# Performance work log

Measured on AMD Instinct MI355X. Metric: run time of the kernel, lower is better.

The kernel has to match this reference:

```python
import jax, jax.numpy as jnp
import numpy as np

B, J, C = 256, 21, 256   # batch, joints, in_dim
H, D = 8, 256            # heads, out_dim (=hidden)
L, K = 2, 8              # layers, knn_k


def _knn_idx(coords, k):
    # coords: (B,J,3). Squared distances give same ordering as cdist p=2.
    d2 = jnp.sum((coords[:, :, None, :] - coords[:, None, :, :]) ** 2, axis=-1)  # (B,J,J)
    order = jnp.argsort(d2, axis=-1)
    return order[..., 1:k + 1]  # drop self -> (B,J,K)


def _mhgat(x, nbr_idx, wq, wk, wv, wp):
    b, j, _ = x.shape
    q = (x @ wq).reshape(b, j, H, D)
    k = (x @ wk).reshape(b, j, H, D)
    v = (x @ wv).reshape(b, j, H, D)
    bi = jnp.arange(b)[:, None, None]
    k_nbr = k[bi, nbr_idx]  # (B,J,K,H,D) gather of neighbor keys
    v_nbr = v[bi, nbr_idx]  # (B,J,K,H,D)
    attn = jnp.einsum('bjhd,bjkhd->bjkh', q, k_nbr) / np.float32(np.sqrt(D))
    attn = jax.nn.leaky_relu(attn, negative_slope=0.2)
    attn = jax.nn.softmax(attn, axis=2)  # over K neighbors
    out = jnp.einsum('bjkh,bjkhd->bjhd', attn, v_nbr).reshape(b, j, H * D)
    return out @ wp  # (B,J,hidden)


def setup_inputs() -> dict:
    key = jax.random.key(0)
    ks = jax.random.split(key, 9)
    s_in = 1.0 / np.sqrt(C)
    s_hd = 1.0 / np.sqrt(H * D)
    s_h = 1.0 / np.sqrt(D)
    joint_feats = jax.random.normal(ks[0], (B, J, C), jnp.float32)
    # layer-stacked weights (in_dim == hidden == 256 so both layers stack)
    wq = jax.random.normal(ks[1], (L, C, H * D), jnp.float32) * s_in
    wk = jax.random.normal(ks[2], (L, C, H * D), jnp.float32) * s_in
    wv = jax.random.normal(ks[3], (L, C, H * D), jnp.float32) * s_in
    wp = jax.random.normal(ks[4], (L, H * D, D), jnp.float32) * s_hd
    ws = jax.random.normal(ks[5], (L, C, D), jnp.float32) * s_in
    wskip0 = jax.random.normal(ks[6], (C, D), jnp.float32) * s_in
    fc_w = jax.random.normal(ks[7], (D, 3), jnp.float32) * s_h
    fc_b = jax.random.normal(ks[8], (3,), jnp.float32) * s_h
    return {"joint_feats": joint_feats, "wq": wq, "wk": wk, "wv": wv,
            "wp": wp, "ws": ws, "wskip0": wskip0, "fc_w": fc_w, "fc_b": fc_b}


def reference(joint_feats, wq, wk, wv, wp, ws, wskip0, fc_w, fc_b):
    h0 = joint_feats
    h = h0
    stats = []
    for l in range(L):
        nbr_idx = _knn_idx(jax.lax.stop_gradient(h[..., :3]), K)  # dynamic kNN graph
        out = _mhgat(h, nbr_idx, wq[l], wk[l], wv[l], wp[l])
        h = jax.nn.relu(out + h @ ws[l] + h0 @ wskip0)
        stats.append(jnp.abs(h).mean())
    coords = h @ fc_w + fc_b
    alphas = jnp.mean(jnp.stack(stats))
    return coords, alphas
```

## Files before the change

### kernel.cpp

```cpp
#include <hip/hip_runtime.h>
#include <hip/hip_bf16.h>
#include <math.h>
#include <type_traits>

namespace {
constexpr int Bb = 256, Jj = 21, Cc = 256, Hh = 8, Dd = 256;
constexpr int Mrows = Bb * Jj;
constexpr int HD    = Hh * Dd;
constexpr int QKVN  = 3 * HD;
constexpr int KNN   = 8;
constexpr int KFUSE = HD + Cc + Cc;

constexpr size_t OFF_QKV   = 0;
constexpr size_t OFF_T     = OFF_QKV   + (size_t)Mrows*QKVN*2;
constexpr size_t OFF_ATT   = OFF_T;
constexpr size_t OFF_GT    = OFF_T     + (size_t)Mrows*HD*4;
constexpr size_t OFF_JFB   = OFF_GT    + (size_t)HD*768*2;
constexpr size_t OFF_JFH   = OFF_JFB   + (size_t)Mrows*Cc*2;
constexpr size_t OFF_JFL   = OFF_JFH   + (size_t)Mrows*Cc*2;
constexpr size_t OFF_JFD   = OFF_JFL   + (size_t)Mrows*Cc*2;
constexpr size_t OFF_H1B   = OFF_JFD   + (size_t)Mrows*Cc*2;
constexpr size_t OFF_H2F   = OFF_H1B   + (size_t)Mrows*Cc*2;
constexpr size_t OFF_WQKVT = OFF_H2F   + (size_t)Mrows*Cc*4;
constexpr size_t OFF_FBT   = OFF_WQKVT + (size_t)2*QKVN*Cc*2;
constexpr size_t OFF_WVP   = OFF_FBT   + (size_t)2*Cc*KFUSE*2;
constexpr size_t OFF_VPROJ = OFF_WVP   + (size_t)Cc*24*4;
constexpr size_t OFF_WSUM  = OFF_VPROJ + (size_t)Mrows*24*4;
constexpr size_t OFF_CRD   = OFF_WSUM  + (size_t)Cc*4*4;
constexpr size_t OFF_NBR0  = OFF_CRD   + (size_t)Mrows*4*4;
constexpr size_t OFF_NBR1  = OFF_NBR0  + (size_t)Mrows*KNN*4;
constexpr size_t OFF_STAT  = OFF_NBR1  + (size_t)Mrows*KNN*4;
}

typedef short short8 __attribute__((ext_vector_type(8)));
typedef _Float16 half8 __attribute__((ext_vector_type(8)));
typedef _Float16 half4v __attribute__((ext_vector_type(4)));
typedef unsigned short u16x8 __attribute__((ext_vector_type(8)));
typedef float f32x4 __attribute__((ext_vector_type(4)));

__device__ __forceinline__ unsigned short f2bf(float x) {
    unsigned int u = __float_as_uint(x);
    u = u + 0x7fffu + ((u >> 16) & 1u);
    return (unsigned short)(u >> 16);
}
__device__ __forceinline__ float bf2f(unsigned short b) {
    return __uint_as_float(((unsigned int)b) << 16);
}

__device__ __forceinline__ void knn_body(int b, const float* __restrict__ src,
                                         int ld, int* __restrict__ nbr,
                                         float (*cs)[3]) {
    int t = threadIdx.x;
    if (t < Jj) {
        const float* p = src + (size_t)(b * Jj + t) * ld;
        cs[t][0] = p[0]; cs[t][1] = p[1]; cs[t][2] = p[2];
    }
    __syncthreads();
    if (t < Jj) {
        float x = cs[t][0], y = cs[t][1], z = cs[t][2];
        float d2[Jj];
        #pragma unroll
        for (int jj = 0; jj < Jj; ++jj) {
            float dx = x - cs[jj][0], dy = y - cs[jj][1], dz = z - cs[jj][2];
            d2[jj] = dx*dx + dy*dy + dz*dz;
        }
        unsigned int used = 0u;
        int out_base = (b * Jj + t) * KNN;
        #pragma unroll
        for (int r = 0; r <= KNN; ++r) {
            int best = -1; float bd = INFINITY;
            #pragma unroll
            for (int jj = 0; jj < Jj; ++jj)
                if (!((used >> jj) & 1u) && d2[jj] < bd) { bd = d2[jj]; best = jj; }
            used |= (1u << best);
            if (r > 0) nbr[out_base + r - 1] = best;
        }
    }
}

__global__ __launch_bounds__(256)
void mega_prep_kernel(const float* __restrict__ jf,
                      const float* __restrict__ wq, const float* __restrict__ wk,
                      const float* __restrict__ wv, const float* __restrict__ wp,
                      const float* __restrict__ wsw, const float* __restrict__ wsk,
                      unsigned short* __restrict__ wqkvT,
                      unsigned short* __restrict__ fbt, float* __restrict__ stats,
                      float* __restrict__ wsum,
                      unsigned short* __restrict__ jfb, _Float16* __restrict__ jfh,
                      _Float16* __restrict__ jfl, _Float16* __restrict__ jfd,
                      _Float16* __restrict__ GT, float* __restrict__ Wvp2,
                      int* __restrict__ nbr0) {
    __shared__ __align__(16) char sm[17408];
    int bid = blockIdx.x;
    int tidx = threadIdx.x;

    if (bid < 4352) {
        const float* src; unsigned short* dst;
        int ldin, ldout, tilesX, tile;
        constexpr size_t CH = (size_t)Cc * HD;
        if (bid < 3072) {
            int op = bid >> 9; tile = bid & 511; tilesX = 64;
            ldin = HD; ldout = Cc;
            const float* s3[3] = {wq, wk, wv};
            src = s3[op % 3] + (size_t)(op / 3) * CH;
            dst = wqkvT + (size_t)(op % 3) * HD * Cc + (size_t)(op / 3) * QKVN * Cc;
        } else if (bid < 4096) {
            int op = (bid - 3072) >> 9; tile = (bid - 3072) & 511; tilesX = 8;
            ldin = Cc; ldout = KFUSE;
            src = wp + (size_t)op * HD * Cc;
            dst = fbt + (size_t)op * Cc * KFUSE;
        } else {
            int q = bid - 4096; int op = q >> 6; tile = q & 63; tilesX = 8;
            ldin = Cc; ldout = KFUSE;
            const float* s4[4] = {wsw, wsw + (size_t)Cc * Cc, wsk, wsk};
            src = s4[op];
            dst = fbt + (size_t)(op & 1) * Cc * KFUSE + HD + (size_t)(op >> 1) * Cc;
        }
        int bx = tile % tilesX, by = tile / tilesX;
        int n0 = bx * 32, k0 = by * 32;
        float (*t)[33] = (float(*)[33])sm;
        int r = tidx >> 3, c4 = (tidx & 7) * 4;
        float4 v = *(const float4*)&src[(size_t)(k0 + r) * ldin + n0 + c4];
        t[r][c4+0] = v.x; t[r][c4+1] = v.y; t[r][c4+2] = v.z; t[r][c4+3] = v.w;
        __syncthreads();
        ushort4 o;
        o.x = f2bf(t[c4+0][r]); o.y = f2bf(t[c4+1][r]);
        o.z = f2bf(t[c4+2][r]); o.w = f2bf(t[c4+3][r]);
        *(ushort4*)&dst[(size_t)(n0 + r) * ldout + k0 + c4] = o;
    } else if (bid == 4352) {
        int e = tidx;
        float4 o;
        o.x = wsw[(size_t)e*Dd + 0] + wsk[(size_t)e*Dd + 0];
        o.y = wsw[(size_t)e*Dd + 1] + wsk[(size_t)e*Dd + 1];
        o.z = wsw[(size_t)e*Dd + 2] + wsk[(size_t)e*Dd + 2];
        o.w = 0.0f;
        *(float4*)&wsum[e*4] = o;
        if (e < 2) stats[e] = 0.0f;
    } else if (bid < 5697) {
        int i = (bid - 4353) * 256 + tidx;
        float4 v = ((const float4*)jf)[i];
        float x[4] = {v.x, v.y, v.z, v.w};
        ushort4 ob; half4v oh, ol, od;
        #pragma unroll
        for (int u = 0; u < 4; ++u) {
            ((unsigned short*)&ob)[u] = f2bf(x[u]);
            _Float16 h = (_Float16)x[u];
            oh[u] = h;
            ol[u] = (_Float16)((x[u] - (float)h) * 16.0f);
            od[u] = (_Float16)(x[u] * 0.0078125f);
        }
        ((ushort4*)jfb)[i] = ob;
        ((half4v*)jfh)[i] = oh;
        ((half4v*)jfl)[i] = ol;
        ((half4v*)jfd)[i] = od;
    } else if (bid < 5825) {
        int q = bid - 5697;
        int h = q >> 4, rem = q & 15;
        int m0 = (rem >> 2) * 64, n0 = (rem & 3) * 64;
        float (*As)[68] = (float(*)[68])sm;
        float (*Ws)[68] = (float(*)[68])(sm + 8704);
        int ty = tidx >> 4, tx = tidx & 15;
        float acc[4][4] = {};
        for (int kb = 0; kb < 256; kb += 32) {
            #pragma unroll
            for (int it = 0; it < 2; ++it) {
                int c = tidx + it * 256;
                int row = c >> 3, col = (c & 7) * 4;
                float4 v = *(const float4*)&wq[(size_t)(m0 + row)*HD + h*256 + kb + col];
                float4 u = *(const float4*)&wk[(size_t)(n0 + row)*HD + h*256 + kb + col];
                As[col+0][row] = v.x; As[col+1][row] = v.y;
                As[col+2][row] = v.z; As[col+3][row] = v.w;
                Ws[col+0][row] = u.x; Ws[col+1][row] = u.y;
                Ws[col+2][row] = u.z; Ws[col+3][row] = u.w;
            }
            __syncthreads();
            #pragma unroll
            for (int kk = 0; kk < 32; ++kk) {
                float4 a = *(const float4*)&As[kk][ty*4];
                float4 b = *(const float4*)&Ws[kk][tx*4];
                float av[4] = {a.x, a.y, a.z, a.w};
                float bv[4] = {b.x, b.y, b.z, b.w};
                #pragma unroll
                for (int i = 0; i < 4; ++i)
                    #pragma unroll
                    for (int j = 0; j < 4; ++j)
                        acc[i][j] += av[i] * bv[j];
            }
            __syncthreads();
        }
        #pragma unroll
        for (int j = 0; j < 4; ++j) {
            int n = h*256 + n0 + tx*4 + j;
            half4v hi, hs, lo;
            #pragma unroll
            for (int i = 0; i < 4; ++i) {
                float g = acc[i][j];
                _Float16 gh = (_Float16)g;
                hi[i] = gh;
                hs[i] = (_Float16)(g * 0.0625f);
                lo[i] = (_Float16)((g - (float)gh) * 128.0f);
            }
            _Float16* base = &GT[(size_t)n*768 + m0 + ty*4];
            *(half4v*)(base)       = hi;
            *(half4v*)(base + 256) = hs;
            *(half4v*)(base + 512) = lo;
        }
    } else if (bid < 5833) {
        int h = bid - 5825;
        float (*wpc)[3] = (float(*)[3])sm;
        int t = tidx;
        const float* p = &wp[(size_t)(h*256 + t) * Cc];
        wpc[t][0] = p[0]; wpc[t][1] = p[1]; wpc[t][2] = p[2];
        __syncthreads();
        const float* vr = &wv[(size_t)t*HD + h*256];
        float a0=0, a1=0, a2=0;
        for (int d = 0; d < 256; ++d) {
            float v = vr[d];
            a0 += v*wpc[d][0]; a1 += v*wpc[d][1]; a2 += v*wpc[d][2];
        }
        float* o = &Wvp2[(size_t)t*24 + h*3];
        o[0]=a0; o[1]=a1; o[2]=a2;
    } else {
        knn_body(bid - 5833, jf, Cc, nbr0, (float(*)[3])sm);
    }
}

template<int BM, int BN, int BK, int NSEG, bool RELU_STATS, bool OUT_BF16, bool F16>
__device__ __forceinline__
void gemm_core(unsigned short* As, unsigned short* Bs, float* red,
               int bm, int bn,
               const unsigned short* __restrict__ A0, int lda0, int klen0,
               const unsigned short* __restrict__ A1, int lda1, int klen1,
               const unsigned short* __restrict__ A2, int lda2, int klen2,
               const unsigned short* __restrict__ Bt, int ldb,
               void* __restrict__ Cv, int ldc, float* __restrict__ stat) {
    constexpr int WM = BM/2, WN = BN/2;
    constexpr int MW = WM/16, NW = WN/16, KW = BK/32;
    constexpr int CHUNKA = BM*BK/8;
    constexpr int CHUNKB = BN*BK/8;
    constexpr int KB8 = BK/8;
    constexpr int SWZ = KB8 - 1;
    using frag = std::conditional_t<F16, half8, short8>;

    int tid = threadIdx.x;
    int wid = tid >> 6, lane = tid & 63;
    int wr = wid >> 1, wc = wid & 1;

    f32x4 acc[MW][NW];
    #pragma unroll
    for (int m = 0; m < MW; ++m)
        #pragma unroll
        for (int n = 0; n < NW; ++n)
            acc[m][n] = (f32x4){0.f, 0.f, 0.f, 0.f};

    const unsigned short* Aseg[3] = {A0, A1, A2};
    const int ldas[3] = {lda0, lda1, lda2};
    const int klens[3] = {klen0, klen1, klen2};

    int kglob = 0;
    for (int seg = 0; seg < NSEG; ++seg) {
        const unsigned short* A = Aseg[seg];
        const int lda = ldas[seg];
        const int klen = klens[seg];
        for (int k0 = 0; k0 < klen; k0 += BK) {
            #pragma unroll
            for (int it = 0; it < CHUNKA/256; ++it) {
                int c = tid + it*256;
                int row = c / KB8;
                int kp = (c % KB8) ^ (row & SWZ);
                __builtin_amdgcn_global_load_lds(
                    (const __attribute__((address_space(1))) unsigned int*)
                        (A + (size_t)(bm + row)*lda + k0 + kp*8),
                    (__attribute__((address_space(3))) unsigned int*)(As + c*8),
                    16, 0, 0);
            }
            #pragma unroll
            for (int it = 0; it < CHUNKB/256; ++it) {
                int c = tid + it*256;
                int row = c / KB8;
                int kp = (c % KB8) ^ (row & SWZ);
                __builtin_amdgcn_global_load_lds(
                    (const __attribute__((address_space(1))) unsigned int*)
                        (Bt + (size_t)(bn + row)*ldb + kglob + k0 + kp*8),
                    (__attribute__((address_space(3))) unsigned int*)(Bs + c*8),
                    16, 0, 0);
            }
            __syncthreads();
            #pragma unroll
            for (int kp = 0; kp < KW; ++kp) {
                frag af[MW], bf[NW];
                int cbase = kp*4 + (lane >> 4);
                #pragma unroll
                for (int m = 0; m < MW; ++m) {
                    int r = wr*WM + m*16 + (lane & 15);
                    af[m] = *(const frag*)&As[r*BK + ((cbase ^ (r & SWZ))*8)];
                }
                #pragma unroll
                for (int n = 0; n < NW; ++n) {
                    int r = wc*WN + n*16 + (lane & 15);
                    bf[n] = *(const frag*)&Bs[r*BK + ((cbase ^ (r & SWZ))*8)];
                }
                #pragma unroll
                for (int m = 0; m < MW; ++m)
                    #pragma unroll
                    for (int n = 0; n < NW; ++n) {
                        if constexpr (F16)
                            acc[m][n] = __builtin_amdgcn_mfma_f32_16x16x32_f16(
                                af[m], bf[n], acc[m][n], 0, 0, 0);
                        else
                            acc[m][n] = __builtin_amdgcn_mfma_f32_16x16x32_bf16(
                                af[m], bf[n], acc[m][n], 0, 0, 0);
                    }
            }
            __syncthreads();
        }
        kglob += klen;
    }

    int cr = (lane >> 4)*4, cc = lane & 15;
    float bsum = 0.0f;
    #pragma unroll
    for (int m = 0; m < MW; ++m)
        #pragma unroll
        for (int n = 0; n < NW; ++n)
            #pragma unroll
            for (int j = 0; j < 4; ++j) {
                float v = acc[m][n][j];
                if (RELU_STATS) { v = fmaxf(v, 0.0f); bsum += v; }
                size_t row = bm + wr*WM + m*16 + cr + j;
                size_t col = bn + wc*WN + n*16 + cc;
                if (OUT_BF16) ((unsigned short*)Cv)[row*ldc + col] = f2bf(v);
                else          ((float*)Cv)[row*ldc + col] = v;
            }
    if (RELU_STATS) {
        #pragma unroll
        for (int sft = 1; sft < 64; sft <<= 1) bsum += __shfl_xor(bsum, sft);
        if (lane == 0) red[wid] = bsum;
        __syncthreads();
        if (tid == 0) atomicAdd(stat, red[0] + red[1] + red[2] + red[3]);
    }
}

__global__ __launch_bounds__(256)
void combo_kernel(const unsigned short* __restrict__ jfb,
                  const unsigned short* __restrict__ wqkvT,
                  unsigned short* __restrict__ QKVb,
                  const _Float16* __restrict__ jfh, const _Float16* __restrict__ jfl,
                  const _Float16* __restrict__ jfd, const _Float16* __restrict__ GT,
                  float* __restrict__ Tm,
                  const float* __restrict__ jf, const float* __restrict__ Wvp2,
                  float* __restrict__ vproj) {
    __shared__ __align__(16) char smem[32784];
    unsigned short* As = (unsigned short*)smem;
    unsigned short* Bs = (unsigned short*)(smem + 16384);
    float* red = (float*)(smem + 32768);
    int x = blockIdx.x, y = blockIdx.y;
    if (y < 48) {
        int lb = x + 42*y;
        int nb = (lb & 7) * 252 + (lb >> 3);
        int sx = nb % 42, sy = nb / 42;
        gemm_core<128,128,64,1,false,true,false>(As, Bs, red, sx*128, sy*128,
            jfb, Cc, Cc, jfb, Cc, 0, jfb, Cc, 0, wqkvT, Cc, QKVb, QKVN, nullptr);
    } else if (y < 64) {
        int lb = x + 42*(y - 48);
        int nb = (lb & 7) * 84 + (lb >> 3);
        int sx = nb / 16, sy = nb % 16;
        gemm_core<128,128,64,3,false,false,true>(As, Bs, red, sx*128, sy*128,
            (const unsigned short*)jfh, Cc, Cc, (const unsigned short*)jfl, Cc, Cc,
            (const unsigned short*)jfd, Cc, Cc, (const unsigned short*)GT, 768,
            Tm, HD, nullptr);
    } else {
        int q = (y - 64) * 42 + x;
        float (*hr)[256] = (float(*)[256])smem;
        float* wl = (float*)(smem + 8192);
        int t = threadIdx.x;
        int j0 = q * 8;
        #pragma unroll
        for (int i = 0; i < 6; ++i)
            *(float4*)&wl[t*4 + i*1024] = *(const float4*)&Wvp2[t*4 + i*1024];
        {
            int r = t >> 5, c = (t & 31) * 8;
            const float* src = &jf[(size_t)(j0 + r)*Cc + c];
            *(float4*)&hr[r][c]   = *(const float4*)src;
            *(float4*)&hr[r][c+4] = *(const float4*)(src + 4);
        }
        __syncthreads();
        int r = t >> 5, o = t & 31;
        if (o < 24) {
            float a = 0.0f;
            for (int e = 0; e < 256; ++e) a += hr[r][e] * wl[e*24 + o];
            vproj[(size_t)(j0 + r)*24 + o] = a;
        }
    }
}

__global__ __launch_bounds__(256)
void qkv1_kernel(const unsigned short* __restrict__ h1b,
                 const unsigned short* __restrict__ wqkvT1,
                 unsigned short* __restrict__ QKVb) {
    __shared__ __align__(16) unsigned short As[128*64];
    __shared__ __align__(16) unsigned short Bs[128*64];
    __shared__ float red[4];
    int lb = blockIdx.x + 42*blockIdx.y;
    int nb = (lb & 7) * 252 + (lb >> 3);
    int sx = nb % 42, sy = nb / 42;
    gemm_core<128,128,64,1,false,true,false>(
        As, Bs, red, sx*128, sy*128,
        h1b, Cc, Cc, h1b, Cc, 0, h1b, Cc, 0, wqkvT1, Cc, QKVb, QKVN, nullptr);
}

template<bool OUT_BF16, bool DO_KNN>
__global__ __launch_bounds__(256)
void fused_kernel(const unsigned short* __restrict__ att,
                  const unsigned short* __restrict__ hseg,
                  const unsigned short* __restrict__ h0seg,
                  const unsigned short* __restrict__ fbtL,
                  void* __restrict__ Cv, float* __restrict__ stat,
                  const float* __restrict__ crd, int* __restrict__ nbr1) {
    __shared__ __align__(16) char smem[16400];
    if (DO_KNN && blockIdx.y >= 4) {
        int b = (blockIdx.y - 4) * 84 + blockIdx.x;
        if (b < Bb) knn_body(b, crd, 4, nbr1, (float(*)[3])smem);
        return;
    }
    unsigned short* As = (unsigned short*)smem;
    unsigned short* Bs = (unsigned short*)(smem + 8192);
    float* red = (float*)(smem + 16384);
    gemm_core<64,64,64,3,true,OUT_BF16,false>(
        As, Bs, red, blockIdx.x*64, blockIdx.y*64,
        att, HD, HD, hseg, Cc, Cc, h0seg, Cc, Cc,
        fbtL, KFUSE, Cv, Cc, stat);
}

__global__ __launch_bounds__(64)
void precise_kernel(const float* __restrict__ T, const float* __restrict__ h0,
                    const int* __restrict__ nbr, const float* __restrict__ vproj,
                    const float* __restrict__ wsum, float* __restrict__ crd) {
    int i = blockIdx.x;
    int b = i / Jj;
    int l = threadIdx.x;
    __shared__ float Ts[8][260];
    __shared__ float nb[8][260];
    __shared__ float hi[256];
    #pragma unroll
    for (int u = 0; u < 8; ++u) {
        int idx = u*64 + l;
        float4 v = *(const float4*)&T[(size_t)i*HD + idx*4];
        int hh = idx >> 6, dd = (idx & 63) * 4;
        *(float4*)&Ts[hh][dd] = v;
    }
    *(float4*)&hi[l*4] = *(const float4*)&h0[(size_t)i*Cc + l*4];
    int kq = l >> 3, s = l & 7;
    int njs = nbr[i*KNN + kq];
    const float* nrow = &h0[(size_t)(b*Jj + njs)*Cc];
    #pragma unroll
    for (int u = 0; u < 8; ++u)
        *(float4*)&nb[kq][(s*8+u)*4] = *(const float4*)&nrow[(s*8+u)*4];
    __syncthreads();

    int k = l >> 3, h = l & 7;
    float sacc = 0;
    #pragma unroll 8
    for (int d = 0; d < 256; d += 4) {
        float4 tv = *(const float4*)&Ts[h][d];
        float4 nv = *(const float4*)&nb[k][d];
        sacc += tv.x*nv.x + tv.y*nv.y + tv.z*nv.z + tv.w*nv.w;
    }
    float sc = sacc * 0.0625f;
    sc = (sc >= 0.0f) ? sc : 0.2f * sc;
    float m = sc;
    m = fmaxf(m, __shfl_xor(m, 8));
    m = fmaxf(m, __shfl_xor(m, 16));
    m = fmaxf(m, __shfl_xor(m, 32));
    float e = expf(sc - m);
    float den = e;
    den += __shfl_xor(den, 8); den += __shfl_xor(den, 16); den += __shfl_xor(den, 32);
    float w = e / den;

    int njk = nbr[i*KNN + k];
    const float* vp = &vproj[(size_t)(b*Jj + njk)*24 + h*3];
    float t0 = w * vp[0], t1 = w * vp[1], t2 = w * vp[2];
    #pragma unroll
    for (int u = 0; u < 4; ++u) {
        int e4 = l*4 + u;
        float hv = hi[e4];
        float4 wv = *(const float4*)&wsum[e4*4];
        t0 += hv * wv.x; t1 += hv * wv.y; t2 += hv * wv.z;
    }
    #pragma unroll
    for (int sft = 1; sft < 64; sft <<= 1) {
        t0 += __shfl_xor(t0, sft); t1 += __shfl_xor(t1, sft); t2 += __shfl_xor(t2, sft);
    }
    if (l == 0) {
        crd[i*4+0] = fmaxf(t0, 0.0f);
        crd[i*4+1] = fmaxf(t1, 0.0f);
        crd[i*4+2] = fmaxf(t2, 0.0f);
        crd[i*4+3] = 0.0f;
    }
}

__global__ __launch_bounds__(64)
void attn_kernel(const unsigned short* __restrict__ QKV,
                 const int* __restrict__ nbr, unsigned short* __restrict__ att) {
    int lb = blockIdx.x;
    int gid = (lb & 7) * (Mrows*4/8) + (lb >> 3);
    int hp = gid & 3, row = gid >> 2, b = row / Jj;
    int lane = threadIdx.x;
    int h = hp*2 + (lane >> 5);
    int d0 = (lane & 31) * 8;

    u16x8 qu = *(const u16x8*)&QKV[(size_t)row*QKVN + h*Dd + d0];
    float qf[8];
    #pragma unroll
    for (int i = 0; i < 8; ++i) qf[i] = bf2f(qu[i]);
    const int* np_ = nbr + row * KNN;

    float sc[KNN]; int nb[KNN];
    #pragma unroll
    for (int k = 0; k < KNN; ++k) {
        int n = np_[k]; nb[k] = n;
        u16x8 ku = *(const u16x8*)&QKV[(size_t)(b*Jj + n)*QKVN + HD + h*Dd + d0];
        float p = 0;
        #pragma unroll
        for (int i = 0; i < 8; ++i) p += qf[i] * bf2f(ku[i]);
        #pragma unroll
        for (int s = 1; s < 32; s <<= 1) p += __shfl_xor(p, s);
        sc[k] = p;
    }
    float mx = -INFINITY;
    #pragma unroll
    for (int k = 0; k < KNN; ++k) {
        float s = sc[k] * 0.0625f;
        s = (s >= 0.0f) ? s : 0.2f * s;
        sc[k] = s; mx = fmaxf(mx, s);
    }
    float den = 0.0f;
    #pragma unroll
    for (int k = 0; k < KNN; ++k) { sc[k] = expf(sc[k] - mx); den += sc[k]; }
    float inv = 1.0f / den;
    float o[8] = {};
    #pragma unroll
    for (int k = 0; k < KNN; ++k) {
        u16x8 vu = *(const u16x8*)&QKV[(size_t)(b*Jj + nb[k])*QKVN + 2*HD + h*Dd + d0];
        float w = sc[k] * inv;
        #pragma unroll
        for (int i = 0; i < 8; ++i) o[i] += w * bf2f(vu[i]);
    }
    u16x8 ou;
    #pragma unroll
    for (int i = 0; i < 8; ++i) ou[i] = f2bf(o[i]);
    *(u16x8*)&att[(size_t)row*HD + h*Dd + d0] = ou;
}

__global__ __launch_bounds__(64)
void final_kernel(const float* __restrict__ h, const float* __restrict__ fcw,
                  const float* __restrict__ fcb, const float* __restrict__ stats,
                  float* __restrict__ out) {
    int row = blockIdx.x, lane = threadIdx.x;
    const float4 hv = *(const float4*)(h + (size_t)row*Cc + lane*4);
    float a0=0, a1=0, a2=0;
    const float hx[4] = {hv.x, hv.y, hv.z, hv.w};
    #pragma unroll
    for (int i = 0; i < 4; ++i) {
        int c = lane*4 + i;
        a0 += hx[i]*fcw[c*3+0]; a1 += hx[i]*fcw[c*3+1]; a2 += hx[i]*fcw[c*3+2];
    }
    #pragma unroll
    for (int s = 32; s > 0; s >>= 1) {
        a0 += __shfl_xor(a0, s); a1 += __shfl_xor(a1, s); a2 += __shfl_xor(a2, s);
    }
    if (lane == 0) {
        out[row*3+0] = a0 + fcb[0];
        out[row*3+1] = a1 + fcb[1];
        out[row*3+2] = a2 + fcb[2];
        if (row == 0)
            out[(size_t)Mrows*3] =
                (stats[0] + stats[1]) * (0.5f / ((float)Mrows * (float)Cc));
    }
}

extern "C" void kernel_launch(void* const* d_in, const int* in_sizes, int n_in,
                              void* d_out, int out_size, void* d_ws, size_t ws_size,
                              hipStream_t stream) {
    (void)in_sizes; (void)n_in; (void)out_size; (void)ws_size;
    const float* jf     = (const float*)d_in[0];
    const float* wq     = (const float*)d_in[1];
    const float* wk     = (const float*)d_in[2];
    const float* wv     = (const float*)d_in[3];
    const float* wp     = (const float*)d_in[4];
    const float* wsw    = (const float*)d_in[5];
    const float* wskip0 = (const float*)d_in[6];
    const float* fcw    = (const float*)d_in[7];
    const float* fcb    = (const float*)d_in[8];
    float* out = (float*)d_out;

    char* wsb = (char*)d_ws;
    unsigned short* QKVb  = (unsigned short*)(wsb + OFF_QKV);
    float*          Tm    = (float*)(wsb + OFF_T);
    unsigned short* attb  = (unsigned short*)(wsb + OFF_ATT);
    _Float16*       GT    = (_Float16*)(wsb + OFF_GT);
    unsigned short* jfb   = (unsigned short*)(wsb + OFF_JFB);
    _Float16*       jfh   = (_Float16*)(wsb + OFF_JFH);
    _Float16*       jfl   = (_Float16*)(wsb + OFF_JFL);
    _Float16*       jfd   = (_Float16*)(wsb + OFF_JFD);
    unsigned short* h1b   = (unsigned short*)(wsb + OFF_H1B);
    float*          h2f   = (float*)(wsb + OFF_H2F);
    unsigned short* wqkvT = (unsigned short*)(wsb + OFF_WQKVT);
    unsigned short* fbt   = (unsigned short*)(wsb + OFF_FBT);
    float*          Wvp   = (float*)(wsb + OFF_WVP);
    float*          vproj = (float*)(wsb + OFF_VPROJ);
    float*          wsum  = (float*)(wsb + OFF_WSUM);
    float*          crd   = (float*)(wsb + OFF_CRD);
    int*            nbr0  = (int*)(wsb + OFF_NBR0);
    int*            nbr1  = (int*)(wsb + OFF_NBR1);
    float*          stats = (float*)(wsb + OFF_STAT);

    mega_prep_kernel<<<6089, 256, 0, stream>>>(jf, wq, wk, wv, wp, wsw, wskip0,
                                               wqkvT, fbt, stats, wsum,
                                               jfb, jfh, jfl, jfd, GT, Wvp, nbr0);
    combo_kernel<<<dim3(42, 80), 256, 0, stream>>>(jfb, wqkvT, QKVb,
                                                   jfh, jfl, jfd, GT, Tm,
                                                   jf, Wvp, vproj);
    precise_kernel<<<Mrows, 64, 0, stream>>>(Tm, jf, nbr0, vproj, wsum, crd);
    attn_kernel<<<Mrows*4, 64, 0, stream>>>(QKVb, nbr0, attb);
    fused_kernel<true, true><<<dim3(84, 8), 256, 0, stream>>>(
        attb, jfb, jfb, fbt, h1b, &stats[0], crd, nbr1);
    qkv1_kernel<<<dim3(42, 48), 256, 0, stream>>>(h1b, wqkvT + (size_t)QKVN*Cc, QKVb);
    attn_kernel<<<Mrows*4, 64, 0, stream>>>(QKVb, nbr1, attb);
    fused_kernel<false, false><<<dim3(84, 4), 256, 0, stream>>>(
        attb, h1b, jfb, fbt + (size_t)Cc*KFUSE, h2f, &stats[1], nullptr, nullptr);
    final_kernel<<<Mrows, 64, 0, stream>>>(h2f, fcw, fcb, stats, out);
}
```

Baseline: 231.7 us.

## Reuse layer-0 precise attention weights and skip Q/K projection GEMM

The layer-0 precise kernel, which already computes softmax attention weights from the T matrix, now stores them to a new buffer. A new attnw_kernel applies those stored weights to the neighbour V rows. This lets the combo kernel compute only the V third of the layer-0 QKV projection, dropping the Q and K GEMM tiles and the per-row score computation in layer-0 attention. It costs an extra write and read of 64 floats per row, and layer 0 now uses fp32-split-derived weights instead of bf16 Q/K scores.

```diff
diff --git a/kernel.cpp b/kernel.cpp
--- a/kernel.cpp
+++ b/kernel.cpp
@@ -29,7 +29,8 @@
 constexpr size_t OFF_CRD   = OFF_WSUM  + (size_t)Cc*4*4;
 constexpr size_t OFF_NBR0  = OFF_CRD   + (size_t)Mrows*4*4;
 constexpr size_t OFF_NBR1  = OFF_NBR0  + (size_t)Mrows*KNN*4;
-constexpr size_t OFF_STAT  = OFF_NBR1  + (size_t)Mrows*KNN*4;
+constexpr size_t OFF_W0    = OFF_NBR1  + (size_t)Mrows*KNN*4;
+constexpr size_t OFF_STAT  = OFF_W0    + (size_t)Mrows*64*4;
 }
 
 typedef short short8 __attribute__((ext_vector_type(8)));
@@ -355,14 +356,15 @@
     unsigned short* Bs = (unsigned short*)(smem + 16384);
     float* red = (float*)(smem + 32768);
     int x = blockIdx.x, y = blockIdx.y;
-    if (y < 48) {
+    if (y < 16) {
         int lb = x + 42*y;
-        int nb = (lb & 7) * 252 + (lb >> 3);
+        int nb = (lb & 7) * 84 + (lb >> 3);
         int sx = nb % 42, sy = nb / 42;
-        gemm_core<128,128,64,1,false,true,false>(As, Bs, red, sx*128, sy*128,
+        gemm_core<128,128,64,1,false,true,false>(As, Bs, red, sx*128,
+            2*HD + sy*128,
             jfb, Cc, Cc, jfb, Cc, 0, jfb, Cc, 0, wqkvT, Cc, QKVb, QKVN, nullptr);
-    } else if (y < 64) {
-        int lb = x + 42*(y - 48);
+    } else if (y < 32) {
+        int lb = x + 42*(y - 16);
         int nb = (lb & 7) * 84 + (lb >> 3);
         int sx = nb / 16, sy = nb % 16;
         gemm_core<128,128,64,3,false,false,true>(As, Bs, red, sx*128, sy*128,
@@ -370,7 +372,7 @@
             (const unsigned short*)jfd, Cc, Cc, (const unsigned short*)GT, 768,
             Tm, HD, nullptr);
     } else {
-        int q = (y - 64) * 42 + x;
+        int q = (y - 32) * 42 + x;
         float (*hr)[256] = (float(*)[256])smem;
         float* wl = (float*)(smem + 8192);
         int t = threadIdx.x;
@@ -435,7 +437,8 @@
 __global__ __launch_bounds__(64)
 void precise_kernel(const float* __restrict__ T, const float* __restrict__ h0,
                     const int* __restrict__ nbr, const float* __restrict__ vproj,
-                    const float* __restrict__ wsum, float* __restrict__ crd) {
+                    const float* __restrict__ wsum, float* __restrict__ crd,
+                    float* __restrict__ W0) {
     int i = blockIdx.x;
     int b = i / Jj;
     int l = threadIdx.x;
@@ -476,6 +479,7 @@
     float den = e;
     den += __shfl_xor(den, 8); den += __shfl_xor(den, 16); den += __shfl_xor(den, 32);
     float w = e / den;
+    W0[(size_t)i*64 + l] = w;
 
     int njk = nbr[i*KNN + k];
     const float* vp = &vproj[(size_t)(b*Jj + njk)*24 + h*3];
@@ -497,6 +501,34 @@
         crd[i*4+2] = fmaxf(t2, 0.0f);
         crd[i*4+3] = 0.0f;
     }
+}
+
+__global__ __launch_bounds__(64)
+void attnw_kernel(const unsigned short* __restrict__ QKV,
+                  const int* __restrict__ nbr, const float* __restrict__ W0,
+                  unsigned short* __restrict__ att) {
+    int lb = blockIdx.x;
+    int gid = (lb & 7) * (Mrows*4/8) + (lb >> 3);
+    int hp = gid & 3, row = gid >> 2, b = row / Jj;
+    int lane = threadIdx.x;
+    int h = hp*2 + (lane >> 5);
+    int d0 = (lane & 31) * 8;
+    const int* np_ = nbr + row * KNN;
+    const float* wr = W0 + (size_t)row*64 + h;
+
+    float o[8] = {};
+    #pragma unroll
+    for (int k = 0; k < KNN; ++k) {
+        float w = wr[k*8];
+        int n = np_[k];
+        u16x8 vu = *(const u16x8*)&QKV[(size_t)(b*Jj + n)*QKVN + 2*HD + h*Dd + d0];
+        #pragma unroll
+        for (int i = 0; i < 8; ++i) o[i] += w * bf2f(vu[i]);
+    }
+    u16x8 ou;
+    #pragma unroll
+    for (int i = 0; i < 8; ++i) ou[i] = f2bf(o[i]);
+    *(u16x8*)&att[(size_t)row*HD + h*Dd + d0] = ou;
 }
 
 __global__ __launch_bounds__(64)
@@ -613,16 +645,17 @@
     float*          crd   = (float*)(wsb + OFF_CRD);
     int*            nbr0  = (int*)(wsb + OFF_NBR0);
     int*            nbr1  = (int*)(wsb + OFF_NBR1);
+    float*          W0    = (float*)(wsb + OFF_W0);
     float*          stats = (float*)(wsb + OFF_STAT);
 
     mega_prep_kernel<<<6089, 256, 0, stream>>>(jf, wq, wk, wv, wp, wsw, wskip0,
                                                wqkvT, fbt, stats, wsum,
                                                jfb, jfh, jfl, jfd, GT, Wvp, nbr0);
-    combo_kernel<<<dim3(42, 80), 256, 0, stream>>>(jfb, wqkvT, QKVb,
+    combo_kernel<<<dim3(42, 48), 256, 0, stream>>>(jfb, wqkvT, QKVb,
                                                    jfh, jfl, jfd, GT, Tm,
                                                    jf, Wvp, vproj);
-    precise_kernel<<<Mrows, 64, 0, stream>>>(Tm, jf, nbr0, vproj, wsum, crd);
-    attn_kernel<<<Mrows*4, 64, 0, stream>>>(QKVb, nbr0, attb);
+    precise_kernel<<<Mrows, 64, 0, stream>>>(Tm, jf, nbr0, vproj, wsum, crd, W0);
+    attnw_kernel<<<Mrows*4, 64, 0, stream>>>(QKVb, nbr0, W0, attb);
     fused_kernel<true, true><<<dim3(84, 8), 256, 0, stream>>>(
         attb, jfb, jfb, fbt, h1b, &stats[0], crd, nbr1);
     qkv1_kernel<<<dim3(42, 48), 256, 0, stream>>>(h1b, wqkvT + (size_t)QKVN*Cc, QKVb);
```

New measurement: 205.1 us. 1.13x faster.

## Fold layer-0 Q/K into precomputed Wq·Wk^T and fuse value aggregation into precise kernel

Applied to the files above, without the earlier changes.

For layer 0, combo_kernel now computes only the V slice of the QKV projection, because the attention scores already come from the precomputed T = h0·(Wq Wk^T) path. The separate layer-0 attn_kernel launch is removed. precise_kernel reuses its softmax weights to aggregate neighbour V rows and writes the attention output itself. This drops two-thirds of the layer-0 QKV GEMM plus one launch. To support it, the ATT buffer gets its own region instead of aliasing T. mega_prep is reordered so the long-running Wq·Wk^T, Wvp and kNN blocks are scheduled first, with a smaller 32x64 tile that gives more blocks. The cost is more per-block work in precise_kernel, whose 64-thread blocks now loop over 8 neighbours × 32 dims of V.

```diff
diff --git a/kernel.cpp b/kernel.cpp
--- a/kernel.cpp
+++ b/kernel.cpp
@@ -13,8 +13,8 @@
 
 constexpr size_t OFF_QKV   = 0;
 constexpr size_t OFF_T     = OFF_QKV   + (size_t)Mrows*QKVN*2;
-constexpr size_t OFF_ATT   = OFF_T;
-constexpr size_t OFF_GT    = OFF_T     + (size_t)Mrows*HD*4;
+constexpr size_t OFF_ATT   = OFF_T     + (size_t)Mrows*HD*4;
+constexpr size_t OFF_GT    = OFF_ATT   + (size_t)Mrows*HD*2;
 constexpr size_t OFF_JFB   = OFF_GT    + (size_t)HD*768*2;
 constexpr size_t OFF_JFH   = OFF_JFB   + (size_t)Mrows*Cc*2;
 constexpr size_t OFF_JFL   = OFF_JFH   + (size_t)Mrows*Cc*2;
@@ -94,23 +94,113 @@
     int bid = blockIdx.x;
     int tidx = threadIdx.x;
 
-    if (bid < 4352) {
+    if (bid < 256) {
+        int h = bid >> 5, rem = bid & 31;
+        int m0 = (rem >> 2) * 32, n0 = (rem & 3) * 64;
+        float (*As)[36] = (float(*)[36])sm;
+        float (*Ws)[68] = (float(*)[68])(sm + 4608);
+        int ty = tidx >> 4, tx = tidx & 15;
+        float acc[2][4] = {};
+        for (int kb = 0; kb < 256; kb += 32) {
+            {
+                int row = tidx >> 3, col = (tidx & 7) * 4;
+                float4 v = *(const float4*)&wq[(size_t)(m0 + row)*HD + h*256 + kb + col];
+                As[col+0][row] = v.x; As[col+1][row] = v.y;
+                As[col+2][row] = v.z; As[col+3][row] = v.w;
+                int row2 = tidx >> 2, col2 = (tidx & 3) * 8;
+                float4 u0 = *(const float4*)&wk[(size_t)(n0 + row2)*HD + h*256 + kb + col2];
+                float4 u1 = *(const float4*)&wk[(size_t)(n0 + row2)*HD + h*256 + kb + col2 + 4];
+                Ws[col2+0][row2] = u0.x; Ws[col2+1][row2] = u0.y;
+                Ws[col2+2][row2] = u0.z; Ws[col2+3][row2] = u0.w;
+                Ws[col2+4][row2] = u1.x; Ws[col2+5][row2] = u1.y;
+                Ws[col2+6][row2] = u1.z; Ws[col2+7][row2] = u1.w;
+            }
+            __syncthreads();
+            #pragma unroll
+            for (int kk = 0; kk < 32; ++kk) {
+                float a0 = As[kk][ty*2], a1 = As[kk][ty*2 + 1];
+                float4 bv = *(const float4*)&Ws[kk][tx*4];
+                float b4[4] = {bv.x, bv.y, bv.z, bv.w};
+                #pragma unroll
+                for (int j = 0; j < 4; ++j) {
+                    acc[0][j] += a0 * b4[j];
+                    acc[1][j] += a1 * b4[j];
+                }
+            }
+            __syncthreads();
+        }
+        #pragma unroll
+        for (int j = 0; j < 4; ++j) {
+            int n = h*256 + n0 + tx*4 + j;
+            float g0 = acc[0][j], g1 = acc[1][j];
+            _Float16 h0_ = (_Float16)g0, h1_ = (_Float16)g1;
+            _Float16* base = &GT[(size_t)n*768 + m0 + ty*2];
+            base[0]   = h0_;                          base[1]   = h1_;
+            base[256] = (_Float16)(g0 * 0.0625f);     base[257] = (_Float16)(g1 * 0.0625f);
+            base[512] = (_Float16)((g0 - (float)h0_) * 128.0f);
+            base[513] = (_Float16)((g1 - (float)h1_) * 128.0f);
+        }
+    } else if (bid < 264) {
+        int h = bid - 256;
+        float (*wpc)[3] = (float(*)[3])sm;
+        int t = tidx;
+        const float* p = &wp[(size_t)(h*256 + t) * Cc];
+        wpc[t][0] = p[0]; wpc[t][1] = p[1]; wpc[t][2] = p[2];
+        __syncthreads();
+        const float* vr = &wv[(size_t)t*HD + h*256];
+        float a0=0, a1=0, a2=0;
+        for (int d = 0; d < 256; ++d) {
+            float v = vr[d];
+            a0 += v*wpc[d][0]; a1 += v*wpc[d][1]; a2 += v*wpc[d][2];
+        }
+        float* o = &Wvp2[(size_t)t*24 + h*3];
+        o[0]=a0; o[1]=a1; o[2]=a2;
+    } else if (bid < 520) {
+        knn_body(bid - 264, jf, Cc, nbr0, (float(*)[3])sm);
+    } else if (bid == 520) {
+        int e = tidx;
+        float4 o;
+        o.x = wsw[(size_t)e*Dd + 0] + wsk[(size_t)e*Dd + 0];
+        o.y = wsw[(size_t)e*Dd + 1] + wsk[(size_t)e*Dd + 1];
+        o.z = wsw[(size_t)e*Dd + 2] + wsk[(size_t)e*Dd + 2];
+        o.w = 0.0f;
+        *(float4*)&wsum[e*4] = o;
+        if (e < 2) stats[e] = 0.0f;
+    } else if (bid < 1865) {
+        int i = (bid - 521) * 256 + tidx;
+        float4 v = ((const float4*)jf)[i];
+        float x[4] = {v.x, v.y, v.z, v.w};
+        ushort4 ob; half4v oh, ol, od;
+        #pragma unroll
+        for (int u = 0; u < 4; ++u) {
+            ((unsigned short*)&ob)[u] = f2bf(x[u]);
+            _Float16 h = (_Float16)x[u];
+            oh[u] = h;
+            ol[u] = (_Float16)((x[u] - (float)h) * 16.0f);
+            od[u] = (_Float16)(x[u] * 0.0078125f);
+        }
+        ((ushort4*)jfb)[i] = ob;
+        ((half4v*)jfh)[i] = oh;
+        ((half4v*)jfl)[i] = ol;
+        ((half4v*)jfd)[i] = od;
+    } else {
+        int tt = bid - 1865;
         const float* src; unsigned short* dst;
         int ldin, ldout, tilesX, tile;
         constexpr size_t CH = (size_t)Cc * HD;
-        if (bid < 3072) {
-            int op = bid >> 9; tile = bid & 511; tilesX = 64;
+        if (tt < 3072) {
+            int op = tt >> 9; tile = tt & 511; tilesX = 64;
             ldin = HD; ldout = Cc;
             const float* s3[3] = {wq, wk, wv};
             src = s3[op % 3] + (size_t)(op / 3) * CH;
             dst = wqkvT + (size_t)(op % 3) * HD * Cc + (size_t)(op / 3) * QKVN * Cc;
-        } else if (bid < 4096) {
-            int op = (bid - 3072) >> 9; tile = (bid - 3072) & 511; tilesX = 8;
+        } else if (tt < 4096) {
+            int op = (tt - 3072) >> 9; tile = (tt - 3072) & 511; tilesX = 8;
             ldin = Cc; ldout = KFUSE;
             src = wp + (size_t)op * HD * Cc;
             dst = fbt + (size_t)op * Cc * KFUSE;
         } else {
-            int q = bid - 4096; int op = q >> 6; tile = q & 63; tilesX = 8;
+            int q = tt - 4096; int op = q >> 6; tile = q & 63; tilesX = 8;
             ldin = Cc; ldout = KFUSE;
             const float* s4[4] = {wsw, wsw + (size_t)Cc * Cc, wsk, wsk};
             src = s4[op];
@@ -127,101 +217,6 @@
         o.x = f2bf(t[c4+0][r]); o.y = f2bf(t[c4+1][r]);
         o.z = f2bf(t[c4+2][r]); o.w = f2bf(t[c4+3][r]);
         *(ushort4*)&dst[(size_t)(n0 + r) * ldout + k0 + c4] = o;
-    } else if (bid == 4352) {
-        int e = tidx;
-        float4 o;
-        o.x = wsw[(size_t)e*Dd + 0] + wsk[(size_t)e*Dd + 0];
-        o.y = wsw[(size_t)e*Dd + 1] + wsk[(size_t)e*Dd + 1];
-        o.z = wsw[(size_t)e*Dd + 2] + wsk[(size_t)e*Dd + 2];
-        o.w = 0.0f;
-        *(float4*)&wsum[e*4] = o;
-        if (e < 2) stats[e] = 0.0f;
-    } else if (bid < 5697) {
-        int i = (bid - 4353) * 256 + tidx;
-        float4 v = ((const float4*)jf)[i];
-        float x[4] = {v.x, v.y, v.z, v.w};
-        ushort4 ob; half4v oh, ol, od;
-        #pragma unroll
-        for (int u = 0; u < 4; ++u) {
-            ((unsigned short*)&ob)[u] = f2bf(x[u]);
-            _Float16 h = (_Float16)x[u];
-            oh[u] = h;
-            ol[u] = (_Float16)((x[u] - (float)h) * 16.0f);
-            od[u] = (_Float16)(x[u] * 0.0078125f);
-        }
-        ((ushort4*)jfb)[i] = ob;
-        ((half4v*)jfh)[i] = oh;
-        ((half4v*)jfl)[i] = ol;
-        ((half4v*)jfd)[i] = od;
-    } else if (bid < 5825) {
-        int q = bid - 5697;
-        int h = q >> 4, rem = q & 15;
-        int m0 = (rem >> 2) * 64, n0 = (rem & 3) * 64;
-        float (*As)[68] = (float(*)[68])sm;
-        float (*Ws)[68] = (float(*)[68])(sm + 8704);
-        int ty = tidx >> 4, tx = tidx & 15;
-        float acc[4][4] = {};
-        for (int kb = 0; kb < 256; kb += 32) {
-            #pragma unroll
-            for (int it = 0; it < 2; ++it) {
-                int c = tidx + it * 256;
-                int row = c >> 3, col = (c & 7) * 4;
-                float4 v = *(const float4*)&wq[(size_t)(m0 + row)*HD + h*256 + kb + col];
-                float4 u = *(const float4*)&wk[(size_t)(n0 + row)*HD + h*256 + kb + col];
-                As[col+0][row] = v.x; As[col+1][row] = v.y;
-                As[col+2][row] = v.z; As[col+3][row] = v.w;
-                Ws[col+0][row] = u.x; Ws[col+1][row] = u.y;
-                Ws[col+2][row] = u.z; Ws[col+3][row] = u.w;
-            }
-            __syncthreads();
-            #pragma unroll
-            for (int kk = 0; kk < 32; ++kk) {
-                float4 a = *(const float4*)&As[kk][ty*4];
-                float4 b = *(const float4*)&Ws[kk][tx*4];
-                float av[4] = {a.x, a.y, a.z, a.w};
-                float bv[4] = {b.x, b.y, b.z, b.w};
-                #pragma unroll
-                for (int i = 0; i < 4; ++i)
-                    #pragma unroll
-                    for (int j = 0; j < 4; ++j)
-                        acc[i][j] += av[i] * bv[j];
-            }
-            __syncthreads();
-        }
-        #pragma unroll
-        for (int j = 0; j < 4; ++j) {
-            int n = h*256 + n0 + tx*4 + j;
-            half4v hi, hs, lo;
-            #pragma unroll
-            for (int i = 0; i < 4; ++i) {
-                float g = acc[i][j];
-                _Float16 gh = (_Float16)g;
-                hi[i] = gh;
-                hs[i] = (_Float16)(g * 0.0625f);
-                lo[i] = (_Float16)((g - (float)gh) * 128.0f);
-            }
-            _Float16* base = &GT[(size_t)n*768 + m0 + ty*4];
-            *(half4v*)(base)       = hi;
-            *(half4v*)(base + 256) = hs;
-            *(half4v*)(base + 512) = lo;
-        }
-    } else if (bid < 5833) {
-        int h = bid - 5825;
-        float (*wpc)[3] = (float(*)[3])sm;
-        int t = tidx;
-        const float* p = &wp[(size_t)(h*256 + t) * Cc];
-        wpc[t][0] = p[0]; wpc[t][1] = p[1]; wpc[t][2] = p[2];
-        __syncthreads();
-        const float* vr = &wv[(size_t)t*HD + h*256];
-        float a0=0, a1=0, a2=0;
-        for (int d = 0; d < 256; ++d) {
-            float v = vr[d];
-            a0 += v*wpc[d][0]; a1 += v*wpc[d][1]; a2 += v*wpc[d][2];
-        }
-        float* o = &Wvp2[(size_t)t*24 + h*3];
-        o[0]=a0; o[1]=a1; o[2]=a2;
-    } else {
-        knn_body(bid - 5833, jf, Cc, nbr0, (float(*)[3])sm);
     }
 }
 
@@ -355,14 +350,15 @@
     unsigned short* Bs = (unsigned short*)(smem + 16384);
     float* red = (float*)(smem + 32768);
     int x = blockIdx.x, y = blockIdx.y;
-    if (y < 48) {
+    if (y < 16) {
         int lb = x + 42*y;
-        int nb = (lb & 7) * 252 + (lb >> 3);
+        int nb = (lb & 7) * 84 + (lb >> 3);
         int sx = nb % 42, sy = nb / 42;
-        gemm_core<128,128,64,1,false,true,false>(As, Bs, red, sx*128, sy*128,
+        gemm_core<128,128,64,1,false,true,false>(As, Bs, red, sx*128,
+            2*HD + sy*128,
             jfb, Cc, Cc, jfb, Cc, 0, jfb, Cc, 0, wqkvT, Cc, QKVb, QKVN, nullptr);
-    } else if (y < 64) {
-        int lb = x + 42*(y - 48);
+    } else if (y < 32) {
+        int lb = x + 42*(y - 16);
         int nb = (lb & 7) * 84 + (lb >> 3);
         int sx = nb / 16, sy = nb % 16;
         gemm_core<128,128,64,3,false,false,true>(As, Bs, red, sx*128, sy*128,
@@ -370,7 +366,7 @@
             (const unsigned short*)jfd, Cc, Cc, (const unsigned short*)GT, 768,
             Tm, HD, nullptr);
     } else {
-        int q = (y - 64) * 42 + x;
+        int q = (y - 32) * 42 + x;
         float (*hr)[256] = (float(*)[256])smem;
         float* wl = (float*)(smem + 8192);
         int t = threadIdx.x;
@@ -435,13 +431,17 @@
 __global__ __launch_bounds__(64)
 void precise_kernel(const float* __restrict__ T, const float* __restrict__ h0,
                     const int* __restrict__ nbr, const float* __restrict__ vproj,
-                    const float* __restrict__ wsum, float* __restrict__ crd) {
+                    const float* __restrict__ wsum,
+                    const unsigned short* __restrict__ QKV,
+                    float* __restrict__ crd, unsigned short* __restrict__ att) {
     int i = blockIdx.x;
     int b = i / Jj;
     int l = threadIdx.x;
     __shared__ float Ts[8][260];
     __shared__ float nb[8][260];
     __shared__ float hi[256];
+    __shared__ float wsL[64];
+    __shared__ int nbs[KNN];
     #pragma unroll
     for (int u = 0; u < 8; ++u) {
         int idx = u*64 + l;
@@ -450,6 +450,7 @@
         *(float4*)&Ts[hh][dd] = v;
     }
     *(float4*)&hi[l*4] = *(const float4*)&h0[(size_t)i*Cc + l*4];
+    if (l < KNN) nbs[l] = nbr[i*KNN + l];
     int kq = l >> 3, s = l & 7;
     int njs = nbr[i*KNN + kq];
     const float* nrow = &h0[(size_t)(b*Jj + njs)*Cc];
@@ -476,8 +477,9 @@
     float den = e;
     den += __shfl_xor(den, 8); den += __shfl_xor(den, 16); den += __shfl_xor(den, 32);
     float w = e / den;
-
-    int njk = nbr[i*KNN + k];
+    wsL[l] = w;
+
+    int njk = nbs[k];
     const float* vp = &vproj[(size_t)(b*Jj + njk)*24 + h*3];
     float t0 = w * vp[0], t1 = w * vp[1], t2 = w * vp[2];
     #pragma unroll
@@ -496,6 +498,30 @@
         crd[i*4+1] = fmaxf(t1, 0.0f);
         crd[i*4+2] = fmaxf(t2, 0.0f);
         crd[i*4+3] = 0.0f;
+    }
+    __syncthreads();
+
+    int h2 = l >> 3, sub = l & 7;
+    float o[32] = {};
+    #pragma unroll
+    for (int kk = 0; kk < KNN; ++kk) {
+        float wk_ = wsL[kk*8 + h2];
+        const unsigned short* vrow =
+            &QKV[(size_t)(b*Jj + nbs[kk])*QKVN + 2*HD + h2*256 + sub*32];
+        #pragma unroll
+        for (int j = 0; j < 4; ++j) {
+            u16x8 v = *(const u16x8*)(vrow + j*8);
+            #pragma unroll
+            for (int u = 0; u < 8; ++u) o[j*8+u] += wk_ * bf2f(v[u]);
+        }
+    }
+    unsigned short* arow = &att[(size_t)i*HD + h2*256 + sub*32];
+    #pragma unroll
+    for (int j = 0; j < 4; ++j) {
+        u16x8 ou;
+        #pragma unroll
+        for (int u = 0; u < 8; ++u) ou[u] = f2bf(o[j*8+u]);
+        *(u16x8*)(arow + j*8) = ou;
     }
 }
 
@@ -615,14 +641,14 @@
     int*            nbr1  = (int*)(wsb + OFF_NBR1);
     float*          stats = (float*)(wsb + OFF_STAT);
 
-    mega_prep_kernel<<<6089, 256, 0, stream>>>(jf, wq, wk, wv, wp, wsw, wskip0,
+    mega_prep_kernel<<<6217, 256, 0, stream>>>(jf, wq, wk, wv, wp, wsw, wskip0,
                                                wqkvT, fbt, stats, wsum,
                                                jfb, jfh, jfl, jfd, GT, Wvp, nbr0);
-    combo_kernel<<<dim3(42, 80), 256, 0, stream>>>(jfb, wqkvT, QKVb,
+    combo_kernel<<<dim3(42, 48), 256, 0, stream>>>(jfb, wqkvT, QKVb,
                                                    jfh, jfl, jfd, GT, Tm,
                                                    jf, Wvp, vproj);
-    precise_kernel<<<Mrows, 64, 0, stream>>>(Tm, jf, nbr0, vproj, wsum, crd);
-    attn_kernel<<<Mrows*4, 64, 0, stream>>>(QKVb, nbr0, attb);
+    precise_kernel<<<Mrows, 64, 0, stream>>>(Tm, jf, nbr0, vproj, wsum,
+                                             QKVb, crd, attb);
     fused_kernel<true, true><<<dim3(84, 8), 256, 0, stream>>>(
         attb, jfb, jfb, fbt, h1b, &stats[0], crd, nbr1);
     qkv1_kernel<<<dim3(42, 48), 256, 0, stream>>>(h1b, wqkvT + (size_t)QKVN*Cc, QKVb);
```

Result: faster. 202.0 us (-12.8%).
